# Performance work log

Measured on AMD Instinct MI355X. Metric: run time of the kernel, lower is better.

Reference implementation:

```python
import jax, jax.numpy as jnp
import numpy as np

N, E, G = 131072, 524288, 4096
IN, H, OUT, ED = 32, 64, 1, 6
DEG_HIST = np.array([0, 13107, 26214, 65536, 26215], dtype=np.float64)
AVG_DEG_LOG = float((np.log(np.arange(len(DEG_HIST)) + 1.0) * DEG_HIST).sum() / DEG_HIST.sum())


def setup_inputs() -> dict:
    key = jax.random.key(0)
    ks = jax.random.split(key, 32)
    def w(k, shape, s=0.1):
        return jax.random.normal(k, shape, jnp.float32) * s
    return {
        "x": jax.random.normal(ks[0], (N, IN), jnp.float32),
        "edge_attr": jax.random.normal(ks[1], (E, ED), jnp.float32),
        "t": jax.random.uniform(ks[2], (G, 1), jnp.float32),
        "p": jax.random.uniform(ks[3], (G, 1), jnp.float32),
        "lin1_W": w(ks[4], (H, IN)), "lin1_b": w(ks[5], (H,)),
        "edge_W": w(ks[6], (3, H, ED)), "edge_b": w(ks[7], (3, H)),
        "pre_W": w(ks[8], (3, H, 3 * H)), "pre_b": w(ks[9], (3, H)),
        "post_W": w(ks[10], (3, H, 13 * H)), "post_b": w(ks[11], (3, H)),
        "clin_W": w(ks[12], (3, H, H)), "clin_b": w(ks[13], (3, H)),
        "bn_g": jnp.ones((3, H), jnp.float32), "bn_b": jnp.zeros((3, H), jnp.float32),
        "lstm_Wih": w(ks[14], (4 * H, 2 * H)), "lstm_Whh": w(ks[15], (4 * H, H)),
        "lstm_bih": w(ks[16], (4 * H,)), "lstm_bhh": w(ks[17], (4 * H,)),
        "mlp_W1": w(ks[18], (64, 2 * H + 2)), "mlp_b1": w(ks[19], (64,)),
        "mlp_W2": w(ks[20], (32, 64)), "mlp_b2": w(ks[21], (32,)),
        "mlp_W3": w(ks[22], (OUT, 32)), "mlp_b3": w(ks[23], (OUT,)),
        "edge_index": jax.random.randint(ks[24], (2, E), 0, N),
        "batch": jnp.sort(jax.random.randint(ks[25], (N,), 0, G)),
    }


def _bn(x, g, b):
    m = x.mean(0)
    v = jnp.mean((x - m) ** 2, 0)  # biased var, as torch BN normalization
    return (x - m) * jax.lax.rsqrt(v + 1e-5) * g + b


def _pna(x, edge_attr, src, dst, eW, eb, prW, prb, poW, pob, lW, lb):
    n = x.shape[0]
    e = edge_attr @ eW.T + eb                                   # [E,H]
    m = jnp.concatenate([x[dst], x[src], e], -1) @ prW.T + prb  # [E,H] message
    cnt = jax.ops.segment_sum(jnp.ones(m.shape[0], m.dtype), dst, n)
    c = jnp.maximum(cnt, 1.0)[:, None]
    mean = jax.ops.segment_sum(m, dst, n) / c
    mean2 = jax.ops.segment_sum(m * m, dst, n) / c
    std = jnp.sqrt(jnp.maximum(mean2 - mean * mean, 0.0) + 1e-5)
    has = (cnt > 0)[:, None]
    mn = jnp.where(has, jax.ops.segment_min(m, dst, n), 0.0)
    mx = jnp.where(has, jax.ops.segment_max(m, dst, n), 0.0)
    agg = jnp.concatenate([mean, mn, mx, std], -1)              # [N,4H]
    logd = jnp.log(jnp.maximum(cnt, 1.0) + 1.0)[:, None]
    out = jnp.concatenate([agg, agg * (logd / AVG_DEG_LOG), agg * (AVG_DEG_LOG / logd)], -1)
    out = jnp.concatenate([x, out], -1) @ poW.T + pob           # post_nn
    return out @ lW.T + lb                                      # final tower-mix lin


def _set2set(x, batch, num_graphs, Wih, Whh, bih, bhh, steps=3):
    hdim = x.shape[1]
    q_star = jnp.zeros((num_graphs, 2 * hdim), x.dtype)
    hs = jnp.zeros((num_graphs, hdim), x.dtype)
    cs = jnp.zeros((num_graphs, hdim), x.dtype)
    for _ in range(steps):
        gates = q_star @ Wih.T + bih + hs @ Whh.T + bhh
        ig, fg, gg, og = jnp.split(gates, 4, -1)
        cs = jax.nn.sigmoid(fg) * cs + jax.nn.sigmoid(ig) * jnp.tanh(gg)
        hs = jax.nn.sigmoid(og) * jnp.tanh(cs)
        e = jnp.sum(x * hs[batch], -1)
        emax = jax.ops.segment_max(e, batch, num_graphs)
        emax = jnp.where(jnp.isfinite(emax), emax, 0.0)
        ex = jnp.exp(e - emax[batch])
        a = ex / (jax.ops.segment_sum(ex, batch, num_graphs)[batch] + 1e-16)
        r = jax.ops.segment_sum(a[:, None] * x, batch, num_graphs)
        q_star = jnp.concatenate([hs, r], -1)
    return q_star


def reference(x, edge_attr, t, p, lin1_W, lin1_b, edge_W, edge_b, pre_W, pre_b, post_W, post_b, clin_W, clin_b, bn_g, bn_b, lstm_Wih, lstm_Whh, lstm_bih, lstm_bhh, mlp_W1, mlp_b1, mlp_W2, mlp_b2, mlp_W3, mlp_b3, edge_index, batch):
    src, dst = edge_index[0], edge_index[1]
    h = jax.nn.relu(x @ lin1_W.T + lin1_b)
    for i in range(3):
        h = _pna(h, edge_attr, src, dst, edge_W[i], edge_b[i], pre_W[i], pre_b[i], post_W[i], post_b[i], clin_W[i], clin_b[i])
        h = jax.nn.relu(_bn(h, bn_g[i], bn_b[i]))
    out = _set2set(h, batch, G, lstm_Wih, lstm_Whh, lstm_bih, lstm_bhh)
    out = jnp.concatenate([out, t, p], 1)
    out = jax.nn.relu(out @ mlp_W1.T + mlp_b1)
    out = jax.nn.relu(out @ mlp_W2.T + mlp_b2)
    out = out @ mlp_W3.T + mlp_b3
    return out.reshape(-1)
```

## Files before the change

### kernel.cpp

```cpp
#include <hip/hip_runtime.h>
#include <hip/hip_bf16.h>
#include <math.h>

#define NN 131072
#define EE 524288
#define GG 4096
#define GCAP 192
#define ACAP 96

typedef __attribute__((ext_vector_type(8))) _Float16 half8;
typedef __attribute__((ext_vector_type(4))) _Float16 half4;
typedef __attribute__((ext_vector_type(4))) float f32x4;

__device__ __forceinline__ float sigmoidf_(float x){ return 1.0f/(1.0f+expf(-x)); }

__global__ void k_gptr(const int* batch, int* gptr){
  int g = blockIdx.x*256+threadIdx.x;
  if (g > GG) return;
  if (g == GG){ gptr[GG]=NN; return; }
  int lo=0, hi=NN;
  while(lo<hi){ int mid=(lo+hi)>>1; if(batch[mid]<g) lo=mid+1; else hi=mid; }
  gptr[g]=lo;
}

__global__ void k_deg(const int* dst, int* deg){
  int e = blockIdx.x*256+threadIdx.x;
  if(e<EE) atomicAdd(&deg[dst[e]], 1);
}

__global__ __launch_bounds__(256) void k_scan_part(const int* deg, int* part){
  __shared__ int red[256];
  int b=blockIdx.x, t=threadIdx.x;
  red[t] = deg[b*256+t];
  __syncthreads();
  for(int off=128; off>0; off>>=1){
    if(t<off) red[t]+=red[t+off];
    __syncthreads();
  }
  if(t==0) part[b]=red[0];
}

__global__ __launch_bounds__(512) void k_scan_top(int* part){
  __shared__ int s[512];
  int t=threadIdx.x;
  s[t]=part[t];
  __syncthreads();
  for(int off=1; off<512; off<<=1){
    int v=s[t];
    int add=(t>=off)?s[t-off]:0;
    __syncthreads();
    s[t]=v+add;
    __syncthreads();
  }
  part[t] = (t==0)?0:s[t-1];
}

__global__ __launch_bounds__(256) void k_scan_apply(const int* deg, const int* part, int* rowptr){
  __shared__ int s[256];
  int b=blockIdx.x, t=threadIdx.x;
  int v0=deg[b*256+t];
  s[t]=v0;
  __syncthreads();
  for(int off=1; off<256; off<<=1){
    int v=s[t];
    int add=(t>=off)?s[t-off]:0;
    __syncthreads();
    s[t]=v+add;
    __syncthreads();
  }
  rowptr[b*256+t] = part[b] + s[t]-v0;
  if(b==511 && t==255) rowptr[NN] = part[b] + s[t];
}

__global__ void k_fill(const int* dst, const int* src, const float* ea,
                       const int* rowptr, int* cursor, int* srcord, float* eaord){
  int e = blockIdx.x*256+threadIdx.x;
  if(e>=EE) return;
  int d = dst[e];
  int pos = atomicAdd(&cursor[d], 1);
  int idx = rowptr[d]+pos;
  srcord[idx] = src[e];
  float2 e0 = *(const float2*)&ea[(size_t)e*6];
  float2 e1 = *(const float2*)&ea[(size_t)e*6+2];
  float2 e2 = *(const float2*)&ea[(size_t)e*6+4];
  *(float2*)&eaord[(size_t)idx*6]   = e0;
  *(float2*)&eaord[(size_t)idx*6+2] = e1;
  *(float2*)&eaord[(size_t)idx*6+4] = e2;
}

__global__ __launch_bounds__(448) void k_prepwf(const float* preW, const float* preb,
      const float* eW, const float* eb, float* WfG, float* bfG){
  int i = blockIdx.x;
  const float* pW = preW + (size_t)i*64*192;
  const float* pb = preb + i*64;
  const float* eWl = eW + (size_t)i*384;
  const float* ebl = eb + i*64;
  int t=threadIdx.x;
  if(t<384){
    int j=t/6, d=t-j*6;
    float a=0.0f;
    for(int k=0;k<64;k++) a += pW[(size_t)j*192+128+k]*eWl[k*6+d];
    WfG[i*384+t]=a;
  } else if(t<448){
    int j=t-384;
    float a=pb[j];
    for(int k=0;k<64;k++) a += pW[(size_t)j*192+128+k]*ebl[k];
    bfG[i*64+j]=a;
  }
}

__global__ void k_prepw16(const float* preW, const float* poW, const float* clW,
                          _Float16* preW16, _Float16* poW16, _Float16* clW16){
  int i = blockIdx.x*256 + threadIdx.x;
  if(i < 36864) preW16[i] = (_Float16)preW[i];
  else if(i < 36864+159744) poW16[i-36864] = (_Float16)poW[i-36864];
  else if(i < 36864+159744+12288) clW16[i-196608] = (_Float16)clW[i-196608];
}

__global__ __launch_bounds__(256) void k_lin1_s(const float* x, const float* W, const float* b, _Float16* y0){
  __shared__ float sW[2112];
  __shared__ float sb[64];
  int t=threadIdx.x;
  for(int i=t;i<2048;i+=256){ int j=i>>5,k=i&31; sW[j*33+k]=W[i]; }
  if(t<64) sb[t]=b[t];
  __syncthreads();
  int w = t>>6, j = t&63;
  for(int it=0; it<32; ++it){
    int n = (blockIdx.x*4 + w) + it*4096;
    float acc = sb[j];
    #pragma unroll 8
    for(int k=0;k<32;k++) acc += x[(size_t)n*32+k]*sW[j*33+k];
    y0[(size_t)n*64+j] = (_Float16)acc;
  }
}

__global__ __launch_bounds__(256) void k_bnmsg(_Float16* hy, const float* sc, const float* sh,
      const _Float16* preW16, _Float16* g12){
  __shared__ _Float16 sAh[64][72];
  __shared__ _Float16 sB0[64][72];
  __shared__ _Float16 sB1[64][72];
  __shared__ float ssc[64], ssh[64];
  int t=threadIdx.x;
  int rb = blockIdx.x*64;
  if(t<64){ ssc[t] = sc? sc[t] : 1.0f; ssh[t] = sh? sh[t] : 0.0f; }
  __syncthreads();
  int sr = t>>2, c0 = (t&3)*16;
  {
    half8 y0 = *(const half8*)&hy[(size_t)(rb+sr)*64 + c0];
    half8 y1 = *(const half8*)&hy[(size_t)(rb+sr)*64 + c0 + 8];
    half8 h0, h1;
    #pragma unroll
    for(int q=0;q<8;q++){
      h0[q] = (_Float16)fmaxf((float)y0[q]*ssc[c0+q]   + ssh[c0+q],   0.0f);
      h1[q] = (_Float16)fmaxf((float)y1[q]*ssc[c0+8+q] + ssh[c0+8+q], 0.0f);
    }
    *(half8*)&sAh[sr][c0]   = h0;
    *(half8*)&sAh[sr][c0+8] = h1;
    *(half8*)&hy[(size_t)(rb+sr)*64 + c0]     = h0;
    *(half8*)&hy[(size_t)(rb+sr)*64 + c0 + 8] = h1;
    const _Float16* w0 = &preW16[(size_t)sr*192 + c0];
    const _Float16* w1 = &preW16[(size_t)sr*192 + 64 + c0];
    *(half8*)&sB0[sr][c0]   = *(const half8*)&w0[0];
    *(half8*)&sB0[sr][c0+8] = *(const half8*)&w0[8];
    *(half8*)&sB1[sr][c0]   = *(const half8*)&w1[0];
    *(half8*)&sB1[sr][c0+8] = *(const half8*)&w1[8];
  }
  __syncthreads();
  int w=t>>6, l=t&63;
  f32x4 acc0[4]={}, acc1[4]={};
  #pragma unroll
  for(int kk=0; kk<2; ++kk){
    half8 a = *(const half8*)&sAh[w*16+(l&15)][kk*32+(l>>4)*8];
    #pragma unroll
    for(int n16=0;n16<4;++n16){
      half8 b0 = *(const half8*)&sB0[n16*16+(l&15)][kk*32+(l>>4)*8];
      half8 b1 = *(const half8*)&sB1[n16*16+(l&15)][kk*32+(l>>4)*8];
      acc0[n16] = __builtin_amdgcn_mfma_f32_16x16x32_f16(a,b0,acc0[n16],0,0,0);
      acc1[n16] = __builtin_amdgcn_mfma_f32_16x16x32_f16(a,b1,acc1[n16],0,0,0);
    }
  }
  #pragma unroll
  for(int n16=0;n16<4;++n16){
    #pragma unroll
    for(int reg=0; reg<4; ++reg){
      int row = w*16+(l>>4)*4+reg;
      int col = n16*16+(l&15);
      g12[(size_t)(rb+row)*128 + col]      = (_Float16)acc0[n16][reg];
      g12[(size_t)(rb+row)*128 + 64 + col] = (_Float16)acc1[n16][reg];
    }
  }
}

__global__ __launch_bounds__(256) void k_gather_f(const int* rowptr, const int* srcord,
      const float* eaord, const _Float16* g12, const float* WfG, const float* bfG,
      _Float16* agg, float* s12, float avgdl){
  __shared__ float sWf[64][6];
  __shared__ float sbf[64];
  __shared__ int   sRow[17];
  __shared__ int   sSrc[GCAP];
  __shared__ float sEA[GCAP][8];
  int t=threadIdx.x;
  int rb = blockIdx.x*16;
  for(int i=t; i<384; i+=256) ((float*)sWf)[i]=WfG[i];
  if(t<64) sbf[t]=bfG[t];
  if(t<17) sRow[t]=rowptr[rb+t];
  __syncthreads();
  int eLo = sRow[0];
  int cnt = sRow[16]-eLo;
  int ccap = (cnt<GCAP)? cnt : GCAP;
  for(int i=t; i<ccap; i+=256) sSrc[i]=srcord[eLo+i];
  for(int i=t; i<ccap; i+=256){
    float2 e0 = *(const float2*)&eaord[(size_t)(eLo+i)*6];
    float2 e1 = *(const float2*)&eaord[(size_t)(eLo+i)*6+2];
    float2 e2 = *(const float2*)&eaord[(size_t)(eLo+i)*6+4];
    *(float2*)&sEA[i][0]=e0;
    *(float2*)&sEA[i][2]=e1;
    *(float2*)&sEA[i][4]=e2;
  }
  __syncthreads();
  int w=t>>6, j=t&63;
  float wf0=sWf[j][0], wf1=sWf[j][1], wf2=sWf[j][2];
  float wf3=sWf[j][3], wf4=sWf[j][4], wf5=sWf[j][5];
  float bfj=sbf[j];
  if(cnt<=GCAP){
    for(int q=0; q<4; ++q){
      int ln = w*4 + q;
      int n  = rb + ln;
      int lo = sRow[ln]-eLo, hi = sRow[ln+1]-eLo;
      float mdst = (float)g12[(size_t)n*128+j] + bfj;
      float sum=0.0f, sq=0.0f, mn=1e30f, mx=-1e30f;
      int r=lo;
      for(; r+1<hi; r+=2){
        int s0=sSrc[r], s1=sSrc[r+1];
        float4 va = *(const float4*)&sEA[r][0];
        float2 vb = *(const float2*)&sEA[r][4];
        float4 wa = *(const float4*)&sEA[r+1][0];
        float2 wb = *(const float2*)&sEA[r+1][4];
        float g0 = (float)g12[(size_t)s0*128+64+j];
        float g1 = (float)g12[(size_t)s1*128+64+j];
        float m0 = mdst + g0 + va.x*wf0 + va.y*wf1 + va.z*wf2 + va.w*wf3 + vb.x*wf4 + vb.y*wf5;
        float m1 = mdst + g1 + wa.x*wf0 + wa.y*wf1 + wa.z*wf2 + wa.w*wf3 + wb.x*wf4 + wb.y*wf5;
        sum += m0; sq += m0*m0; mn = fminf(mn,m0); mx = fmaxf(mx,m0);
        sum += m1; sq += m1*m1; mn = fminf(mn,m1); mx = fmaxf(mx,m1);
      }
      if(r<hi){
        int s0=sSrc[r];
        float4 va = *(const float4*)&sEA[r][0];
        float2 vb = *(const float2*)&sEA[r][4];
        float g0 = (float)g12[(size_t)s0*128+64+j];
        float m0 = mdst + g0 + va.x*wf0 + va.y*wf1 + va.z*wf2 + va.w*wf3 + vb.x*wf4 + vb.y*wf5;
        sum += m0; sq += m0*m0; mn = fminf(mn,m0); mx = fmaxf(mx,m0);
      }
      int c = hi-lo;
      float cm = fmaxf((float)c, 1.0f);
      float mean = sum/cm;
      float sd = sqrtf(fmaxf(sq/cm - mean*mean, 0.0f)+1e-5f);
      bool has = c>0;
      size_t base = (size_t)n*256;
      agg[base+j]     = (_Float16)mean;
      agg[base+64+j]  = (_Float16)(has?mn:0.0f);
      agg[base+128+j] = (_Float16)(has?mx:0.0f);
      agg[base+192+j] = (_Float16)sd;
      if(j==0){ float ld=logf(cm+1.0f); s12[n*2]=ld/avgdl; s12[n*2+1]=avgdl/ld; }
    }
  } else {
    for(int q=0; q<4; ++q){
      int ln = w*4 + q;
      int n  = rb + ln;
      int lo = sRow[ln], hi = sRow[ln+1];
      float mdst = (float)g12[(size_t)n*128+j] + bfj;
      float sum=0.0f, sq=0.0f, mn=1e30f, mx=-1e30f;
      int idx=lo;
      for(; idx+1<hi; idx+=2){
        int r0 = idx-eLo, r1 = r0+1;
        int s0, s1;
        float e00,e01,e02,e03,e04,e05, e10,e11,e12,e13,e14,e15;
        if(r1 < GCAP){
          s0=sSrc[r0]; s1=sSrc[r1];
          float4 va = *(const float4*)&sEA[r0][0];
          float2 vb = *(const float2*)&sEA[r0][4];
          float4 wa = *(const float4*)&sEA[r1][0];
          float2 wb = *(const float2*)&sEA[r1][4];
          e00=va.x; e01=va.y; e02=va.z; e03=va.w; e04=vb.x; e05=vb.y;
          e10=wa.x; e11=wa.y; e12=wa.z; e13=wa.w; e14=wb.x; e15=wb.y;
        } else {
          s0=srcord[idx]; s1=srcord[idx+1];
          e00=eaord[(size_t)idx*6+0]; e01=eaord[(size_t)idx*6+1]; e02=eaord[(size_t)idx*6+2];
          e03=eaord[(size_t)idx*6+3]; e04=eaord[(size_t)idx*6+4]; e05=eaord[(size_t)idx*6+5];
          e10=eaord[(size_t)(idx+1)*6+0]; e11=eaord[(size_t)(idx+1)*6+1]; e12=eaord[(size_t)(idx+1)*6+2];
          e13=eaord[(size_t)(idx+1)*6+3]; e14=eaord[(size_t)(idx+1)*6+4]; e15=eaord[(size_t)(idx+1)*6+5];
        }
        float g0 = (float)g12[(size_t)s0*128+64+j];
        float g1 = (float)g12[(size_t)s1*128+64+j];
        float m0 = mdst + g0 + e00*wf0 + e01*wf1 + e02*wf2 + e03*wf3 + e04*wf4 + e05*wf5;
        float m1 = mdst + g1 + e10*wf0 + e11*wf1 + e12*wf2 + e13*wf3 + e14*wf4 + e15*wf5;
        sum += m0; sq += m0*m0; mn = fminf(mn,m0); mx = fmaxf(mx,m0);
        sum += m1; sq += m1*m1; mn = fminf(mn,m1); mx = fmaxf(mx,m1);
      }
      if(idx<hi){
        int r0 = idx-eLo;
        int s0; float e00,e01,e02,e03,e04,e05;
        if(r0 < GCAP){
          s0=sSrc[r0];
          float4 va = *(const float4*)&sEA[r0][0];
          float2 vb = *(const float2*)&sEA[r0][4];
          e00=va.x; e01=va.y; e02=va.z; e03=va.w; e04=vb.x; e05=vb.y;
        } else {
          s0=srcord[idx];
          e00=eaord[(size_t)idx*6+0]; e01=eaord[(size_t)idx*6+1]; e02=eaord[(size_t)idx*6+2];
          e03=eaord[(size_t)idx*6+3]; e04=eaord[(size_t)idx*6+4]; e05=eaord[(size_t)idx*6+5];
        }
        float g0 = (float)g12[(size_t)s0*128+64+j];
        float m0 = mdst + g0 + e00*wf0 + e01*wf1 + e02*wf2 + e03*wf3 + e04*wf4 + e05*wf5;
        sum += m0; sq += m0*m0; mn = fminf(mn,m0); mx = fmaxf(mx,m0);
      }
      int c = hi-lo;
      float cm = fmaxf((float)c, 1.0f);
      float mean = sum/cm;
      float sd = sqrtf(fmaxf(sq/cm - mean*mean, 0.0f)+1e-5f);
      bool has = c>0;
      size_t base = (size_t)n*256;
      agg[base+j]     = (_Float16)mean;
      agg[base+64+j]  = (_Float16)(has?mn:0.0f);
      agg[base+128+j] = (_Float16)(has?mx:0.0f);
      agg[base+192+j] = (_Float16)sd;
      if(j==0){ float ld=logf(cm+1.0f); s12[n*2]=ld/avgdl; s12[n*2+1]=avgdl/ld; }
    }
  }
}

__global__ __launch_bounds__(256) void k_tower_mfma(_Float16* hy, const _Float16* agg, const float* s12,
        const _Float16* poW16, const float* pob, const _Float16* clW16, const float* clb, float* part){
  __shared__ _Float16 sAh[64][72];
  __shared__ _Float16 sB0[64][72];
  __shared__ _Float16 sB1[64][72];
  __shared__ _Float16 sB2[64][72];
  __shared__ float sS[128];
  __shared__ float sredS[16][64];
  __shared__ float sredQ[16][64];
  int t = threadIdx.x;
  int rb = blockIdx.x*64;
  int w = t>>6, l = t&63;
  int sr = t>>2, c0 = (t&3)*16;
  if (t < 128) sS[t] = s12[(size_t)(rb+(t>>1))*2 + (t&1)];
  f32x4 hacc[4]={}, z0a[4]={}, z1a[4]={}, z2a[4]={};
  auto stageTo = [&](_Float16 (*dst)[72], const _Float16* wr){
    *(half8*)&dst[sr][c0]   = *(const half8*)&wr[0];
    *(half8*)&dst[sr][c0+8] = *(const half8*)&wr[8];
  };
  auto mfma8 = [&](f32x4* acc, _Float16 (*B)[72]){
    #pragma unroll
    for (int kk=0; kk<2; ++kk){
      half8 a = *(const half8*)&sAh[w*16 + (l&15)][kk*32 + (l>>4)*8];
      #pragma unroll
      for (int n16=0; n16<4; ++n16){
        half8 b = *(const half8*)&B[n16*16 + (l&15)][kk*32 + (l>>4)*8];
        acc[n16] = __builtin_amdgcn_mfma_f32_16x16x32_f16(a, b, acc[n16], 0, 0, 0);
      }
    }
  };
  stageTo(sAh, &hy[(size_t)(rb+sr)*64 + c0]);
  stageTo(sB0, &poW16[(size_t)sr*832 + c0]);
  __syncthreads();
  mfma8(hacc, sB0);
  for (int kt=0; kt<4; ++kt){
    __syncthreads();
    stageTo(sAh, &agg[(size_t)(rb+sr)*256 + kt*64 + c0]);
    stageTo(sB0, &poW16[(size_t)sr*832 + 64 + kt*64 + c0]);
    stageTo(sB1, &poW16[(size_t)sr*832 + 64 + 256 + kt*64 + c0]);
    stageTo(sB2, &poW16[(size_t)sr*832 + 64 + 512 + kt*64 + c0]);
    __syncthreads();
    mfma8(z0a, sB0);
    mfma8(z1a, sB1);
    mfma8(z2a, sB2);
  }
  __syncthreads();
  #pragma unroll
  for (int n16=0; n16<4; ++n16){
    #pragma unroll
    for (int reg=0; reg<4; ++reg){
      int row = w*16 + (l>>4)*4 + reg;
      int col = n16*16 + (l&15);
      float s1v = sS[row*2], s2v = sS[row*2+1];
      float v = hacc[n16][reg] + z0a[n16][reg] + s1v*z1a[n16][reg] + s2v*z2a[n16][reg] + pob[col];
      sAh[row][col] = (_Float16)v;
    }
  }
  stageTo(sB0, &clW16[(size_t)sr*64 + c0]);
  __syncthreads();
  f32x4 cacc[4] = {};
  mfma8(cacc, sB0);
  float cs_[4], cq_[4];
  #pragma unroll
  for (int n16=0; n16<4; ++n16){ cs_[n16]=0.0f; cq_[n16]=0.0f; }
  #pragma unroll
  for (int n16=0; n16<4; ++n16){
    #pragma unroll
    for (int reg=0; reg<4; ++reg){
      int row = w*16 + (l>>4)*4 + reg;
      int col = n16*16 + (l&15);
      float v = cacc[n16][reg] + clb[col];
      hy[(size_t)(rb+row)*64 + col] = (_Float16)v;
      cs_[n16] += v; cq_[n16] += v*v;
    }
  }
  int slot = w*4 + (l>>4);
  #pragma unroll
  for (int n16=0; n16<4; ++n16){
    int col = n16*16 + (l&15);
    sredS[slot][col] = cs_[n16];
    sredQ[slot][col] = cq_[n16];
  }
  __syncthreads();
  if (t < 64){
    float S=0.0f, Q=0.0f;
    #pragma unroll
    for(int q2=0;q2<16;q2++){ S += sredS[q2][t]; Q += sredQ[q2][t]; }
    part[(size_t)blockIdx.x*128 + t]      = S;
    part[(size_t)blockIdx.x*128 + 64 + t] = Q;
  }
}

__global__ __launch_bounds__(128) void k_bnred(const float* part, double* part2){
  int b = blockIdx.x, t = threadIdx.x;
  double s = 0.0;
  #pragma unroll 8
  for(int r=0;r<32;r++) s += (double)part[(size_t)(b*32+r)*128 + t];
  part2[(size_t)b*128 + t] = s;
}

__global__ __launch_bounds__(64) void k_bnfin(const double* part2, const float* g, const float* bb,
                                              float* sc, float* sh){
  int c = threadIdx.x;
  double S=0.0, Q=0.0;
  for(int b=0;b<64;b++){
    S += part2[(size_t)b*128 + c];
    Q += part2[(size_t)b*128 + 64 + c];
  }
  double mean = S/(double)NN;
  double var  = Q/(double)NN - mean*mean;
  float scale = g[c] * (float)(1.0/sqrt(var+1e-5));
  sc[c]=scale;
  sh[c]=bb[c] - (float)mean*scale;
}

__global__ void k_bnapply16(_Float16* hy, const float* sc, const float* sh){
  int idx = blockIdx.x*256+threadIdx.x;
  for(int i=idx; i<NN*8; i+=256*2048){
    int c0 = (i&7)*8;
    half8 v = *(const half8*)&hy[(size_t)i*8];
    half8 r;
    #pragma unroll
    for(int q=0;q<8;q++) r[q]=(_Float16)fmaxf((float)v[q]*sc[c0+q]+sh[c0+q],0.0f);
    *(half8*)&hy[(size_t)i*8] = r;
  }
}

__global__ __launch_bounds__(256) void k_lstm_lit(float* A, float* cs,
      const float* Wih, const float* Whh, const float* bih, const float* bhh){
  __shared__ float sA[8][128];
  __shared__ float sg[8][256];
  int t=threadIdx.x;
  int g0 = blockIdx.x*8;
  for(int i=t;i<1024;i+=256) sA[i>>7][i&127] = A[(size_t)(g0+(i>>7))*128 + (i&127)];
  __syncthreads();
  float bb2 = bih[t]+bhh[t];
  float acc[8];
  #pragma unroll
  for(int g=0;g<8;g++) acc[g]=bb2;
  for(int k=0;k<128;k+=4){
    float4 wv = *(const float4*)&Wih[(size_t)t*128+k];
    #pragma unroll
    for(int g=0;g<8;g++)
      acc[g] += wv.x*sA[g][k] + wv.y*sA[g][k+1] + wv.z*sA[g][k+2] + wv.w*sA[g][k+3];
  }
  for(int k=0;k<64;k+=4){
    float4 wv = *(const float4*)&Whh[(size_t)t*64+k];
    #pragma unroll
    for(int g=0;g<8;g++)
      acc[g] += wv.x*sA[g][k] + wv.y*sA[g][k+1] + wv.z*sA[g][k+2] + wv.w*sA[g][k+3];
  }
  #pragma unroll
  for(int g=0;g<8;g++) sg[g][t]=acc[g];
  __syncthreads();
  for(int i=t;i<512;i+=256){
    int g=i>>6, j=i&63;
    float ig=sg[g][j], fg=sg[g][64+j], gg=sg[g][128+j], og=sg[g][192+j];
    float c = sigmoidf_(fg)*cs[(size_t)(g0+g)*64+j] + sigmoidf_(ig)*tanhf(gg);
    float hv = sigmoidf_(og)*tanhf(c);
    cs[(size_t)(g0+g)*64+j]=c;
    A[(size_t)(g0+g)*128+j]=hv;
  }
}

__global__ __launch_bounds__(64) void k_attn_f(const _Float16* h16, const int* gptr, float* A){
  __shared__ _Float16 sH[ACAP][66];
  __shared__ float sE[ACAP];
  __shared__ float saq[64];
  int g=blockIdx.x, j=threadIdx.x;
  int lo=gptr[g], hi=gptr[g+1];
  int cnt=hi-lo;
  if(cnt<=0){ A[(size_t)g*128+64+j]=0.0f; return; }
  float aq = A[(size_t)g*128+j];
  saq[j]=aq;
  if(cnt<=ACAP){
    for(int i=0;i<cnt;++i) sH[i][j] = h16[(size_t)(lo+i)*64+j];
    __syncthreads();
    for(int i=j;i<cnt;i+=64){
      float v=0.0f;
      for(int k=0;k<64;k++) v += (float)sH[i][k]*saq[k];
      sE[i]=v;
    }
    __syncthreads();
    float mx=-1e30f;
    for(int i=j;i<cnt;i+=64) mx=fmaxf(mx,sE[i]);
    #pragma unroll
    for(int m=32;m;m>>=1) mx=fmaxf(mx,__shfl_xor(mx,m,64));
    float s=0.0f;
    for(int i=j;i<cnt;i+=64) s+=expf(sE[i]-mx);
    #pragma unroll
    for(int m=32;m;m>>=1) s+=__shfl_xor(s,m,64);
    float inv=1.0f/(s+1e-16f);
    for(int i=j;i<cnt;i+=64) sE[i]=expf(sE[i]-mx)*inv;
    __syncthreads();
    float r=0.0f;
    for(int i=0;i<cnt;++i) r += sE[i]*(float)sH[i][j];
    A[(size_t)g*128+64+j]=r;
  } else {
    float mx=-1e30f;
    for(int n=lo;n<hi;++n){
      float v=(float)h16[(size_t)n*64+j]*aq;
      #pragma unroll
      for(int m=32;m;m>>=1) v+=__shfl_xor(v,m,64);
      mx=fmaxf(mx,v);
    }
    float s=0.0f;
    for(int n=lo;n<hi;++n){
      float v=(float)h16[(size_t)n*64+j]*aq;
      #pragma unroll
      for(int m=32;m;m>>=1) v+=__shfl_xor(v,m,64);
      s+=expf(v-mx);
    }
    float inv=1.0f/(s+1e-16f);
    float r=0.0f;
    for(int n=lo;n<hi;++n){
      float v=(float)h16[(size_t)n*64+j]*aq;
      #pragma unroll
      for(int m=32;m;m>>=1) v+=__shfl_xor(v,m,64);
      r+=expf(v-mx)*inv*(float)h16[(size_t)n*64+j];
    }
    A[(size_t)g*128+64+j]=r;
  }
}

__global__ __launch_bounds__(64) void k_mlp(const float* A, const float* tt, const float* pp,
     const float* W1,const float* b1,const float* W2,const float* b2,const float* W3,const float* b3,
     float* out){
  __shared__ float si[130]; __shared__ float o1[64]; __shared__ float o2[32];
  int g=blockIdx.x, t=threadIdx.x;
  si[t]=A[g*128+t]; si[64+t]=A[g*128+64+t];
  if(t==0){ si[128]=tt[g]; si[129]=pp[g]; }
  __syncthreads();
  float a=b1[t];
  for(int k=0;k<130;k++) a+=W1[t*130+k]*si[k];
  o1[t]=fmaxf(a,0.0f);
  __syncthreads();
  if(t<32){
    float a2=b2[t];
    #pragma unroll 4
    for(int k=0;k<64;k++) a2+=W2[t*64+k]*o1[k];
    o2[t]=fmaxf(a2,0.0f);
  }
  __syncthreads();
  float v = (t<32)? o2[t]*W3[t] : 0.0f;
  #pragma unroll
  for(int m=32;m;m>>=1) v+=__shfl_xor(v,m,64);
  if(t==0) out[g]=v+b3[0];
}

extern "C" void kernel_launch(void* const* d_in, const int* in_sizes, int n_in,
                              void* d_out, int out_size, void* d_ws, size_t ws_size,
                              hipStream_t stream) {
  static const int want[28] = {4194304,3145728,4096,4096,2048,64,1152,192,36864,192,
                               159744,192,12288,192,192,192,32768,16384,256,256,
                               8320,64,2048,32,32,1,1048576,131072};
  if (n_in != 28 || out_size != GG) return;
  for (int i=0;i<28;i++) if (in_sizes[i] != want[i]) return;

  const float* x     = (const float*)d_in[0];
  const float* ea    = (const float*)d_in[1];
  const float* tt    = (const float*)d_in[2];
  const float* pp    = (const float*)d_in[3];
  const float* lin1W = (const float*)d_in[4];
  const float* lin1b = (const float*)d_in[5];
  const float* edgeW = (const float*)d_in[6];
  const float* edgeb = (const float*)d_in[7];
  const float* preW  = (const float*)d_in[8];
  const float* preb  = (const float*)d_in[9];
  const float* postW = (const float*)d_in[10];
  const float* postb = (const float*)d_in[11];
  const float* clinW = (const float*)d_in[12];
  const float* clinb = (const float*)d_in[13];
  const float* bng   = (const float*)d_in[14];
  const float* bnb   = (const float*)d_in[15];
  const float* Wih   = (const float*)d_in[16];
  const float* Whh   = (const float*)d_in[17];
  const float* bih   = (const float*)d_in[18];
  const float* bhh   = (const float*)d_in[19];
  const float* W1    = (const float*)d_in[20];
  const float* b1    = (const float*)d_in[21];
  const float* W2    = (const float*)d_in[22];
  const float* b2    = (const float*)d_in[23];
  const float* W3    = (const float*)d_in[24];
  const float* b3    = (const float*)d_in[25];
  const int*   eidx  = (const int*)d_in[26];
  const int*   batch = (const int*)d_in[27];
  const int* esrc = eidx;
  const int* edst = eidx + EE;

  char* w = (char*)d_ws;
  auto alloc = [&](size_t bytes)->char*{ char* p=w; w += ((bytes+255)/256)*256; return p; };
  _Float16* agg  = (_Float16*)alloc((size_t)NN*256*2);
  _Float16* g12  = (_Float16*)alloc((size_t)NN*128*2);
  _Float16* hy   = (_Float16*)alloc((size_t)NN*64*2);
  int*   deg    = (int*)alloc((size_t)NN*4);
  int*   cursor = (int*)alloc((size_t)NN*4);
  int*   rowptr = (int*)alloc((size_t)(NN+1)*4);
  int*   spart  = (int*)alloc(512*4);
  int*   srcord = (int*)alloc((size_t)EE*4);
  float* eaord  = (float*)alloc((size_t)EE*6*4);
  float* s12   = (float*)alloc((size_t)NN*2*4);
  float* part  = (float*)alloc((size_t)2048*128*4);
  double* part2 = (double*)alloc((size_t)64*128*8);
  float* bnsc  = (float*)alloc(256);
  float* bnsh  = (float*)alloc(256);
  float* WfG   = (float*)alloc(3*384*4);
  float* bfG   = (float*)alloc(3*64*4);
  _Float16* preW16 = (_Float16*)alloc(36864*2);
  _Float16* poW16  = (_Float16*)alloc(159744*2);
  _Float16* clW16  = (_Float16*)alloc(12288*2);
  int*   gptr  = (int*)alloc((GG+1)*4);
  size_t need = (size_t)(w - (char*)d_ws);
  if (need > ws_size) return;
  float* A    = (float*)g12;
  float* cs   = (float*)g12 + (size_t)GG*128;

  double num = 13107.0*log(2.0)+26214.0*log(3.0)+65536.0*log(4.0)+26215.0*log(5.0);
  float avgdl = (float)(num/131072.0);

  hipMemsetAsync(deg, 0, (size_t)NN*4*2, stream);
  hipLaunchKernelGGL(k_deg, dim3(2048), dim3(256), 0, stream, edst, deg);
  hipLaunchKernelGGL(k_scan_part, dim3(512), dim3(256), 0, stream, deg, spart);
  hipLaunchKernelGGL(k_scan_top, dim3(1), dim3(512), 0, stream, spart);
  hipLaunchKernelGGL(k_scan_apply, dim3(512), dim3(256), 0, stream, deg, spart, rowptr);
  hipLaunchKernelGGL(k_fill, dim3(2048), dim3(256), 0, stream, edst, esrc, ea, rowptr, cursor, srcord, eaord);

  hipLaunchKernelGGL(k_gptr, dim3(17), dim3(256), 0, stream, batch, gptr);
  hipLaunchKernelGGL(k_prepwf, dim3(3), dim3(448), 0, stream, preW, preb, edgeW, edgeb, WfG, bfG);
  hipLaunchKernelGGL(k_prepw16, dim3(817), dim3(256), 0, stream, preW, postW, clinW, preW16, poW16, clW16);
  hipLaunchKernelGGL(k_lin1_s, dim3(1024), dim3(256), 0, stream, x, lin1W, lin1b, hy);

  for (int i = 0; i < 3; ++i){
    const float* sc_i = (i==0)? nullptr : bnsc;
    const float* sh_i = (i==0)? nullptr : bnsh;
    hipLaunchKernelGGL(k_bnmsg, dim3(2048), dim3(256), 0, stream, hy, sc_i, sh_i,
        preW16 + (size_t)i*12288, g12);
    hipLaunchKernelGGL(k_gather_f, dim3(8192), dim3(256), 0, stream, rowptr, srcord, eaord, g12,
        WfG + (size_t)i*384, bfG + (size_t)i*64, agg, s12, avgdl);
    hipLaunchKernelGGL(k_tower_mfma, dim3(2048), dim3(256), 0, stream, hy, agg, s12,
        poW16 + (size_t)i*53248, postb + i*64, clW16 + (size_t)i*4096, clinb + i*64, part);
    hipLaunchKernelGGL(k_bnred, dim3(64), dim3(128), 0, stream, part, part2);
    hipLaunchKernelGGL(k_bnfin, dim3(1), dim3(64), 0, stream, part2, bng + i*64, bnb + i*64, bnsc, bnsh);
  }
  hipLaunchKernelGGL(k_bnapply16, dim3(2048), dim3(256), 0, stream, hy, bnsc, bnsh);

  hipMemsetAsync(A, 0, (size_t)GG*128*4, stream);
  hipMemsetAsync(cs, 0, (size_t)GG*64*4, stream);
  for (int s = 0; s < 3; ++s){
    hipLaunchKernelGGL(k_lstm_lit, dim3(512), dim3(256), 0, stream, A, cs, Wih, Whh, bih, bhh);
    hipLaunchKernelGGL(k_attn_f, dim3(GG), dim3(64), 0, stream, hy, gptr, A);
  }
  hipLaunchKernelGGL(k_mlp, dim3(GG), dim3(64), 0, stream, A, tt, pp, W1, b1, W2, b2, W3, b3, (float*)d_out);
}
```

Measured before the change: 534.5 us.

## Load MFMA weight operands directly from global and double-buffer A tiles

In the message and tower kernels, weight B-operands are now read straight from global memory (L1/L2-cached) into registers instead of being staged through shared memory. This cuts LDS use and barriers. The tower kernel also double-buffers the activation tiles, so the next agg slice is staged while the current one is multiplied. The cost is more uncoalesced global loads of the small weight matrices per wave, which rely on cache hits.

```diff
diff --git a/kernel.cpp b/kernel.cpp
--- a/kernel.cpp
+++ b/kernel.cpp
@@ -137,8 +137,6 @@
 __global__ __launch_bounds__(256) void k_bnmsg(_Float16* hy, const float* sc, const float* sh,
       const _Float16* preW16, _Float16* g12){
   __shared__ _Float16 sAh[64][72];
-  __shared__ _Float16 sB0[64][72];
-  __shared__ _Float16 sB1[64][72];
   __shared__ float ssc[64], ssh[64];
   int t=threadIdx.x;
   int rb = blockIdx.x*64;
@@ -158,12 +156,6 @@
     *(half8*)&sAh[sr][c0+8] = h1;
     *(half8*)&hy[(size_t)(rb+sr)*64 + c0]     = h0;
     *(half8*)&hy[(size_t)(rb+sr)*64 + c0 + 8] = h1;
-    const _Float16* w0 = &preW16[(size_t)sr*192 + c0];
-    const _Float16* w1 = &preW16[(size_t)sr*192 + 64 + c0];
-    *(half8*)&sB0[sr][c0]   = *(const half8*)&w0[0];
-    *(half8*)&sB0[sr][c0+8] = *(const half8*)&w0[8];
-    *(half8*)&sB1[sr][c0]   = *(const half8*)&w1[0];
-    *(half8*)&sB1[sr][c0+8] = *(const half8*)&w1[8];
   }
   __syncthreads();
   int w=t>>6, l=t&63;
@@ -173,8 +165,9 @@
     half8 a = *(const half8*)&sAh[w*16+(l&15)][kk*32+(l>>4)*8];
     #pragma unroll
     for(int n16=0;n16<4;++n16){
-      half8 b0 = *(const half8*)&sB0[n16*16+(l&15)][kk*32+(l>>4)*8];
-      half8 b1 = *(const half8*)&sB1[n16*16+(l&15)][kk*32+(l>>4)*8];
+      const _Float16* bp = &preW16[(size_t)(n16*16+(l&15))*192 + kk*32 + (l>>4)*8];
+      half8 b0 = *(const half8*)&bp[0];
+      half8 b1 = *(const half8*)&bp[64];
       acc0[n16] = __builtin_amdgcn_mfma_f32_16x16x32_f16(a,b0,acc0[n16],0,0,0);
       acc1[n16] = __builtin_amdgcn_mfma_f32_16x16x32_f16(a,b1,acc1[n16],0,0,0);
     }
@@ -331,10 +324,8 @@
 
 __global__ __launch_bounds__(256) void k_tower_mfma(_Float16* hy, const _Float16* agg, const float* s12,
         const _Float16* poW16, const float* pob, const _Float16* clW16, const float* clb, float* part){
-  __shared__ _Float16 sAh[64][72];
-  __shared__ _Float16 sB0[64][72];
-  __shared__ _Float16 sB1[64][72];
-  __shared__ _Float16 sB2[64][72];
+  __shared__ _Float16 sA0[64][72];
+  __shared__ _Float16 sA1[64][72];
   __shared__ float sS[128];
   __shared__ float sredS[16][64];
   __shared__ float sredQ[16][64];
@@ -344,37 +335,49 @@
   int sr = t>>2, c0 = (t&3)*16;
   if (t < 128) sS[t] = s12[(size_t)(rb+(t>>1))*2 + (t&1)];
   f32x4 hacc[4]={}, z0a[4]={}, z1a[4]={}, z2a[4]={};
-  auto stageTo = [&](_Float16 (*dst)[72], const _Float16* wr){
-    *(half8*)&dst[sr][c0]   = *(const half8*)&wr[0];
-    *(half8*)&dst[sr][c0+8] = *(const half8*)&wr[8];
+  auto stageA = [&](_Float16 (*dst)[72], const _Float16* src){
+    *(half8*)&dst[sr][c0]   = *(const half8*)&src[0];
+    *(half8*)&dst[sr][c0+8] = *(const half8*)&src[8];
   };
-  auto mfma8 = [&](f32x4* acc, _Float16 (*B)[72]){
+  auto mfmaH = [&](_Float16 (*A)[72]){
     #pragma unroll
     for (int kk=0; kk<2; ++kk){
-      half8 a = *(const half8*)&sAh[w*16 + (l&15)][kk*32 + (l>>4)*8];
+      half8 a = *(const half8*)&A[w*16 + (l&15)][kk*32 + (l>>4)*8];
       #pragma unroll
       for (int n16=0; n16<4; ++n16){
-        half8 b = *(const half8*)&B[n16*16 + (l&15)][kk*32 + (l>>4)*8];
-        acc[n16] = __builtin_amdgcn_mfma_f32_16x16x32_f16(a, b, acc[n16], 0, 0, 0);
+        const _Float16* bp = &poW16[(size_t)(n16*16+(l&15))*832 + kk*32 + (l>>4)*8];
+        hacc[n16] = __builtin_amdgcn_mfma_f32_16x16x32_f16(a, *(const half8*)&bp[0], hacc[n16], 0, 0, 0);
       }
     }
   };
-  stageTo(sAh, &hy[(size_t)(rb+sr)*64 + c0]);
-  stageTo(sB0, &poW16[(size_t)sr*832 + c0]);
-  __syncthreads();
-  mfma8(hacc, sB0);
-  for (int kt=0; kt<4; ++kt){
-    __syncthreads();
-    stageTo(sAh, &agg[(size_t)(rb+sr)*256 + kt*64 + c0]);
-    stageTo(sB0, &poW16[(size_t)sr*832 + 64 + kt*64 + c0]);
-    stageTo(sB1, &poW16[(size_t)sr*832 + 64 + 256 + kt*64 + c0]);
-    stageTo(sB2, &poW16[(size_t)sr*832 + 64 + 512 + kt*64 + c0]);
-    __syncthreads();
-    mfma8(z0a, sB0);
-    mfma8(z1a, sB1);
-    mfma8(z2a, sB2);
-  }
-  __syncthreads();
+  auto mfma3 = [&](_Float16 (*A)[72], int off){
+    #pragma unroll
+    for (int kk=0; kk<2; ++kk){
+      half8 a = *(const half8*)&A[w*16 + (l&15)][kk*32 + (l>>4)*8];
+      #pragma unroll
+      for (int n16=0; n16<4; ++n16){
+        const _Float16* bp = &poW16[(size_t)(n16*16+(l&15))*832 + kk*32 + (l>>4)*8];
+        z0a[n16] = __builtin_amdgcn_mfma_f32_16x16x32_f16(a, *(const half8*)&bp[off],     z0a[n16], 0, 0, 0);
+        z1a[n16] = __builtin_amdgcn_mfma_f32_16x16x32_f16(a, *(const half8*)&bp[off+256], z1a[n16], 0, 0, 0);
+        z2a[n16] = __builtin_amdgcn_mfma_f32_16x16x32_f16(a, *(const half8*)&bp[off+512], z2a[n16], 0, 0, 0);
+      }
+    }
+  };
+  stageA(sA0, &hy[(size_t)(rb+sr)*64 + c0]);
+  __syncthreads();
+  stageA(sA1, &agg[(size_t)(rb+sr)*256 + 0*64 + c0]);
+  mfmaH(sA0);
+  __syncthreads();
+  stageA(sA0, &agg[(size_t)(rb+sr)*256 + 1*64 + c0]);
+  mfma3(sA1, 64 + 0*64);
+  __syncthreads();
+  stageA(sA1, &agg[(size_t)(rb+sr)*256 + 2*64 + c0]);
+  mfma3(sA0, 64 + 1*64);
+  __syncthreads();
+  stageA(sA0, &agg[(size_t)(rb+sr)*256 + 3*64 + c0]);
+  mfma3(sA1, 64 + 2*64);
+  __syncthreads();
+  mfma3(sA0, 64 + 3*64);
   #pragma unroll
   for (int n16=0; n16<4; ++n16){
     #pragma unroll
@@ -383,13 +386,22 @@
       int col = n16*16 + (l&15);
       float s1v = sS[row*2], s2v = sS[row*2+1];
       float v = hacc[n16][reg] + z0a[n16][reg] + s1v*z1a[n16][reg] + s2v*z2a[n16][reg] + pob[col];
-      sAh[row][col] = (_Float16)v;
-    }
-  }
-  stageTo(sB0, &clW16[(size_t)sr*64 + c0]);
+      sA1[row][col] = (_Float16)v;
+    }
+  }
   __syncthreads();
   f32x4 cacc[4] = {};
-  mfma8(cacc, sB0);
+  {
+    #pragma unroll
+    for (int kk=0; kk<2; ++kk){
+      half8 a = *(const half8*)&sA1[w*16 + (l&15)][kk*32 + (l>>4)*8];
+      #pragma unroll
+      for (int n16=0; n16<4; ++n16){
+        const _Float16* bp = &clW16[(size_t)(n16*16+(l&15))*64 + kk*32 + (l>>4)*8];
+        cacc[n16] = __builtin_amdgcn_mfma_f32_16x16x32_f16(a, *(const half8*)&bp[0], cacc[n16], 0, 0, 0);
+      }
+    }
+  }
   float cs_[4], cq_[4];
   #pragma unroll
   for (int n16=0; n16<4; ++n16){ cs_[n16]=0.0f; cq_[n16]=0.0f; }
```

Result: slower. 804.9 us (+50.6%).
